# Kernel tuning notes

Hardware: AMD Instinct MI355X
Metric: run time of the kernel (lower is better)

Reference implementation:

```python
import jax, jax.numpy as jnp
import numpy as np

N, NOBJ, M, H, W = 512, 16, 8192, 128, 128


def _rand_rotations(key, n):
    A = jax.random.normal(key, (n, 3, 3), dtype=jnp.float32)
    q, r = jnp.linalg.qr(A)
    q = q * jnp.sign(jnp.diagonal(r, axis1=-2, axis2=-1))[:, None, :]
    det = jnp.linalg.det(q)  # +-1; flip first column if det == -1
    q = q.at[:, :, 0].multiply(det[:, None])
    return q


def setup_inputs() -> dict:
    key = jax.random.key(0)
    ks = jax.random.split(key, 10)
    obj_id = jax.random.randint(ks[0], (N,), 0, NOBJ, dtype=jnp.int32)
    # realistic pinhole intrinsics (pixels), slight per-sample jitter
    base_K = jnp.array([[600.0, 0.0, 64.0], [0.0, 600.0, 64.0], [0.0, 0.0, 1.0]], jnp.float32)
    cam_K = base_K[None] + jax.random.normal(ks[1], (N, 3, 3)) * jnp.array(
        [[5.0, 0.0, 1.0], [0.0, 5.0, 1.0], [0.0, 0.0, 0.0]], jnp.float32)
    gt_R = _rand_rotations(ks[2], N)
    # small rotational perturbation for pred
    pred_R = _rand_rotations(ks[3], N) @ gt_R
    gt_t = jnp.concatenate([jax.random.normal(ks[4], (N, 2)) * 20.0,
                            500.0 + jax.random.uniform(ks[4], (N, 1)) * 300.0], axis=-1)
    pred_t = gt_t + jax.random.normal(ks[5], (N, 3)) * 5.0
    mesh_points = jax.random.normal(ks[6], (NOBJ, M, 3)) * 50.0  # mm-scale meshes
    diameters = 150.0 + jax.random.uniform(ks[7], (NOBJ,)) * 150.0
    gt_coord_3d_roi = jax.random.normal(ks[8], (N, 3, H, W)) * 50.0
    gt_mask_vis_roi = jax.random.bernoulli(ks[9], 0.4, (N, 1, H, W))
    return dict(obj_id=obj_id, cam_K=cam_K, gt_cam_R_m2c=gt_R, gt_cam_t_m2c=gt_t,
                pred_cam_R_m2c=pred_R, pred_cam_t_m2c=pred_t,
                gt_coord_3d_roi=gt_coord_3d_roi, gt_mask_vis_roi=gt_mask_vis_roi,
                mesh_points=mesh_points, diameters=diameters)


def _project(K, x):
    # K: [N,3,3], x: [N,...,3] -> pixel coords [N,...,2]
    h = jnp.einsum('nij,n...j->n...i', K, x)
    return h[..., :2] / h[..., 2:3]


def reference(obj_id, cam_K, gt_cam_R_m2c, gt_cam_t_m2c, pred_cam_R_m2c,
              pred_cam_t_m2c, gt_coord_3d_roi, gt_mask_vis_roi, mesh_points, diameters):
    # RE (degrees)
    R_diff = pred_cam_R_m2c @ jnp.swapaxes(gt_cam_R_m2c, -2, -1)
    trace = R_diff[..., 0, 0] + R_diff[..., 1, 1] + R_diff[..., 2, 2]
    re = jnp.arccos((jnp.clip(trace, -1.0, 3.0) - 1.0) * 0.5) * (180.0 / jnp.pi)
    # TE (cm)
    te = jnp.linalg.norm(pred_cam_t_m2c - gt_cam_t_m2c, axis=-1) * 100.0
    # ADD: mean distance between transformed mesh points, / diameter
    pts = mesh_points[obj_id]                      # [N,M,3]
    dR = pred_cam_R_m2c - gt_cam_R_m2c
    dt = pred_cam_t_m2c - gt_cam_t_m2c
    diff = jnp.einsum('nij,nmj->nmi', dR, pts) + dt[:, None, :]
    ad = jnp.linalg.norm(diff, axis=-1).mean(axis=-1) / diameters[obj_id]
    # PROJ: mean projected distance over mesh points
    xp = jnp.einsum('nij,nmj->nmi', pred_cam_R_m2c, pts) + pred_cam_t_m2c[:, None, :]
    xg = jnp.einsum('nij,nmj->nmi', gt_cam_R_m2c, pts) + gt_cam_t_m2c[:, None, :]
    pj = jnp.linalg.norm(_project(cam_K, xp) - _project(cam_K, xg), axis=-1).mean(axis=-1)
    # PROJ-visible: same over visible ROI pixels (masked mean instead of ragged gather)
    verts = jnp.transpose(gt_coord_3d_roi, (0, 2, 3, 1))  # [N,H,W,3]
    vp = jnp.einsum('nij,nhwj->nhwi', pred_cam_R_m2c, verts) + pred_cam_t_m2c[:, None, None, :]
    vg = jnp.einsum('nij,nhwj->nhwi', gt_cam_R_m2c, verts) + gt_cam_t_m2c[:, None, None, :]
    d = jnp.linalg.norm(_project(cam_K, vp) - _project(cam_K, vg), axis=-1)  # [N,H,W]
    mask = gt_mask_vis_roi[:, 0].astype(d.dtype)
    pv = (d * mask).sum(axis=(1, 2)) / jnp.maximum(mask.sum(axis=(1, 2)), 1.0)
    return re, te, ad, pj, pv
```

## Files before the change

kernel.cpp:

```cpp
#include <hip/hip_runtime.h>
#include <math.h>

#define NS   512
#define NOBJ 16
#define MPTS 8192
#define HH   128
#define WW   128
#define HW   (HH * WW)
#define BLOCK 1024
#define NWAVE (BLOCK / 64)

__device__ __forceinline__ float frcp(float x)  { return __builtin_amdgcn_rcpf(x); }
__device__ __forceinline__ float fsqrt(float x) { return __builtin_amdgcn_sqrtf(x); }

__global__ __launch_bounds__(BLOCK) void score_kernel(
    const int*   __restrict__ obj_id,
    const float* __restrict__ cam_K,
    const float* __restrict__ gt_R,
    const float* __restrict__ gt_t,
    const float* __restrict__ pr_R,
    const float* __restrict__ pr_t,
    const float* __restrict__ coord,
    const int*   __restrict__ mask,
    const float* __restrict__ mesh,
    const float* __restrict__ diam,
    float*       __restrict__ out)
{
    const int n   = blockIdx.x;
    const int tid = threadIdx.x;

    float K[9], Rg[9], Rp[9], tg[3], tp[3];
#pragma unroll
    for (int i = 0; i < 9; ++i) {
        K[i]  = cam_K[n * 9 + i];
        Rg[i] = gt_R [n * 9 + i];
        Rp[i] = pr_R [n * 9 + i];
    }
#pragma unroll
    for (int i = 0; i < 3; ++i) {
        tg[i] = gt_t[n * 3 + i];
        tp[i] = pr_t[n * 3 + i];
    }
    const int   obj = obj_id[n];
    const float dia = diam[obj];

    float dR[9], dt[3];
#pragma unroll
    for (int i = 0; i < 9; ++i) dR[i] = Rp[i] - Rg[i];
#pragma unroll
    for (int i = 0; i < 3; ++i) dt[i] = tp[i] - tg[i];

    float Ap[9], Ag[9], bp[3], bg[3];
#pragma unroll
    for (int r = 0; r < 3; ++r) {
#pragma unroll
        for (int c = 0; c < 3; ++c) {
            Ap[r * 3 + c] = K[r * 3 + 0] * Rp[0 * 3 + c]
                          + K[r * 3 + 1] * Rp[1 * 3 + c]
                          + K[r * 3 + 2] * Rp[2 * 3 + c];
            Ag[r * 3 + c] = K[r * 3 + 0] * Rg[0 * 3 + c]
                          + K[r * 3 + 1] * Rg[1 * 3 + c]
                          + K[r * 3 + 2] * Rg[2 * 3 + c];
        }
        bp[r] = K[r * 3 + 0] * tp[0] + K[r * 3 + 1] * tp[1] + K[r * 3 + 2] * tp[2];
        bg[r] = K[r * 3 + 0] * tg[0] + K[r * 3 + 1] * tg[1] + K[r * 3 + 2] * tg[2];
    }

    float s_ad = 0.0f, s_pj = 0.0f;

    const float4* mp4 = (const float4*)(mesh + (size_t)obj * MPTS * 3);
#pragma unroll
    for (int it = 0; it < MPTS / (BLOCK * 4); ++it) {
        const int k = it * BLOCK + tid;
        const float4 f0 = mp4[k * 3 + 0];
        const float4 f1 = mp4[k * 3 + 1];
        const float4 f2 = mp4[k * 3 + 2];
        const float px[4] = {f0.x, f0.w, f1.z, f2.y};
        const float py[4] = {f0.y, f1.x, f1.w, f2.z};
        const float pz[4] = {f0.z, f1.y, f2.x, f2.w};
#pragma unroll
        for (int j = 0; j < 4; ++j) {
            const float x = px[j], y = py[j], z = pz[j];
            const float dx = fmaf(dR[0], x, fmaf(dR[1], y, fmaf(dR[2], z, dt[0])));
            const float dy = fmaf(dR[3], x, fmaf(dR[4], y, fmaf(dR[5], z, dt[1])));
            const float dz = fmaf(dR[6], x, fmaf(dR[7], y, fmaf(dR[8], z, dt[2])));
            s_ad += fsqrt(fmaf(dx, dx, fmaf(dy, dy, dz * dz)));
            const float hpx = fmaf(Ap[0], x, fmaf(Ap[1], y, fmaf(Ap[2], z, bp[0])));
            const float hpy = fmaf(Ap[3], x, fmaf(Ap[4], y, fmaf(Ap[5], z, bp[1])));
            const float hpz = fmaf(Ap[6], x, fmaf(Ap[7], y, fmaf(Ap[8], z, bp[2])));
            const float hgx = fmaf(Ag[0], x, fmaf(Ag[1], y, fmaf(Ag[2], z, bg[0])));
            const float hgy = fmaf(Ag[3], x, fmaf(Ag[4], y, fmaf(Ag[5], z, bg[1])));
            const float hgz = fmaf(Ag[6], x, fmaf(Ag[7], y, fmaf(Ag[8], z, bg[2])));
            const float iwp = frcp(hpz), iwg = frcp(hgz);
            const float du = fmaf(hpx, iwp, -hgx * iwg);
            const float dv = fmaf(hpy, iwp, -hgy * iwg);
            s_pj += fsqrt(fmaf(du, du, dv * dv));
        }
    }

    const float* cx = coord + (size_t)n * 3 * HW;
    const int*   mk = mask + (size_t)n * HW;
    const float4* cx4 = (const float4*)cx;
    const float4* cy4 = (const float4*)(cx + HW);
    const float4* cz4 = (const float4*)(cx + 2 * HW);
    const int4*   mk4 = (const int4*)mk;

    float s_pv = 0.0f, s_m = 0.0f;
#pragma unroll
    for (int it = 0; it < HW / 4 / BLOCK; ++it) {
        const int p = it * BLOCK + tid;
        const float4 vx = cx4[p];
        const float4 vy = cy4[p];
        const float4 vz = cz4[p];
        const int4   mm = mk4[p];

        const float xs[4] = {vx.x, vx.y, vx.z, vx.w};
        const float ys[4] = {vy.x, vy.y, vy.z, vy.w};
        const float zs[4] = {vz.x, vz.y, vz.z, vz.w};
        const int   ms[4] = {mm.x, mm.y, mm.z, mm.w};

#pragma unroll
        for (int j = 0; j < 4; ++j) {
            const float x = xs[j], y = ys[j], z = zs[j];
            const float hpx = fmaf(Ap[0], x, fmaf(Ap[1], y, fmaf(Ap[2], z, bp[0])));
            const float hpy = fmaf(Ap[3], x, fmaf(Ap[4], y, fmaf(Ap[5], z, bp[1])));
            const float hpz = fmaf(Ap[6], x, fmaf(Ap[7], y, fmaf(Ap[8], z, bp[2])));
            const float hgx = fmaf(Ag[0], x, fmaf(Ag[1], y, fmaf(Ag[2], z, bg[0])));
            const float hgy = fmaf(Ag[3], x, fmaf(Ag[4], y, fmaf(Ag[5], z, bg[1])));
            const float hgz = fmaf(Ag[6], x, fmaf(Ag[7], y, fmaf(Ag[8], z, bg[2])));
            const float iwp = frcp(hpz), iwg = frcp(hgz);
            const float du = fmaf(hpx, iwp, -hgx * iwg);
            const float dv = fmaf(hpy, iwp, -hgy * iwg);
            const float d  = fsqrt(fmaf(du, du, dv * dv));
            const float fm = (ms[j] != 0) ? 1.0f : 0.0f;
            s_pv += d * fm;
            s_m  += fm;
        }
    }

    float vals[4] = {s_ad, s_pj, s_pv, s_m};
#pragma unroll
    for (int k = 0; k < 4; ++k) {
#pragma unroll
        for (int off = 32; off > 0; off >>= 1)
            vals[k] += __shfl_down(vals[k], off, 64);
    }

    __shared__ float red[4][NWAVE];
    const int wave = tid >> 6;
    const int lane = tid & 63;
    if (lane == 0) {
#pragma unroll
        for (int k = 0; k < 4; ++k) red[k][wave] = vals[k];
    }
    __syncthreads();

    if (tid == 0) {
        float tot[4];
#pragma unroll
        for (int k = 0; k < 4; ++k) {
            float s = 0.0f;
#pragma unroll
            for (int w = 0; w < NWAVE; ++w) s += red[k][w];
            tot[k] = s;
        }

        float trace = 0.0f;
#pragma unroll
        for (int i = 0; i < 9; ++i) trace += Rp[i] * Rg[i];
        trace = fminf(fmaxf(trace, -1.0f), 3.0f);
        const float re = acosf((trace - 1.0f) * 0.5f) * (180.0f / 3.14159265358979323846f);
        const float te = sqrtf(dt[0] * dt[0] + dt[1] * dt[1] + dt[2] * dt[2]) * 100.0f;

        out[0 * NS + n] = re;
        out[1 * NS + n] = te;
        out[2 * NS + n] = tot[0] * (1.0f / MPTS) / dia;
        out[3 * NS + n] = tot[1] * (1.0f / MPTS);
        out[4 * NS + n] = tot[2] / fmaxf(tot[3], 1.0f);
    }
}

extern "C" void kernel_launch(void* const* d_in, const int* in_sizes, int n_in,
                              void* d_out, int out_size, void* d_ws, size_t ws_size,
                              hipStream_t stream) {
    const int*   obj_id = (const int*)  d_in[0];
    const float* cam_K  = (const float*)d_in[1];
    const float* gt_R   = (const float*)d_in[2];
    const float* gt_t   = (const float*)d_in[3];
    const float* pr_R   = (const float*)d_in[4];
    const float* pr_t   = (const float*)d_in[5];
    const float* coord  = (const float*)d_in[6];
    const int*   mask   = (const int*)  d_in[7];
    const float* mesh   = (const float*)d_in[8];
    const float* diam   = (const float*)d_in[9];
    float* out = (float*)d_out;

    score_kernel<<<NS, BLOCK, 0, stream>>>(obj_id, cam_K, gt_R, gt_t, pr_R, pr_t,
                                           coord, mask, mesh, diam, out);
}
```

Baseline: 190.5 us.

## Split each sample across four smaller blocks with a second reduction kernel

Each sample's mesh and ROI work is split across four 256-thread blocks, giving 2048 blocks instead of 512 blocks of 1024 threads. Partial sums go to workspace, and a small second kernel combines them and writes the AD/PROJ/PROJ-visible outputs. Per-sample constants are made wave-uniform with readfirstlane so they can live in scalar registers. The intent is better occupancy, load balance and tail behaviour across CUs, at the cost of an extra launch and a workspace round trip.

Result: no change. 192.0 us (+0.8%).

```diff
diff --git a/kernel.cpp b/kernel.cpp
--- a/kernel.cpp
+++ b/kernel.cpp
@@ -1,19 +1,23 @@
 #include <hip/hip_runtime.h>
 #include <math.h>
 
-#define NS   512
-#define NOBJ 16
-#define MPTS 8192
-#define HH   128
-#define WW   128
-#define HW   (HH * WW)
-#define BLOCK 1024
+#define NS    512
+#define NOBJ  16
+#define MPTS  8192
+#define HH    128
+#define WW    128
+#define HW    (HH * WW)
+#define BLOCK 256
+#define SPLIT 4
 #define NWAVE (BLOCK / 64)
 
 __device__ __forceinline__ float frcp(float x)  { return __builtin_amdgcn_rcpf(x); }
 __device__ __forceinline__ float fsqrt(float x) { return __builtin_amdgcn_sqrtf(x); }
-
-__global__ __launch_bounds__(BLOCK) void score_kernel(
+__device__ __forceinline__ float rfl(float x) {
+    return __int_as_float(__builtin_amdgcn_readfirstlane(__float_as_int(x)));
+}
+
+__global__ __launch_bounds__(BLOCK) void score_partial(
     const int*   __restrict__ obj_id,
     const float* __restrict__ cam_K,
     const float* __restrict__ gt_R,
@@ -23,10 +27,12 @@
     const float* __restrict__ coord,
     const int*   __restrict__ mask,
     const float* __restrict__ mesh,
-    const float* __restrict__ diam,
+    float*       __restrict__ ws,
     float*       __restrict__ out)
 {
-    const int n   = blockIdx.x;
+    const int b   = blockIdx.x;
+    const int n   = b >> 2;
+    const int c   = b & (SPLIT - 1);
     const int tid = threadIdx.x;
 
     float K[9], Rg[9], Rp[9], tg[3], tp[3];
@@ -41,37 +47,44 @@
         tg[i] = gt_t[n * 3 + i];
         tp[i] = pr_t[n * 3 + i];
     }
-    const int   obj = obj_id[n];
-    const float dia = diam[obj];
-
-    float dR[9], dt[3];
-#pragma unroll
-    for (int i = 0; i < 9; ++i) dR[i] = Rp[i] - Rg[i];
-#pragma unroll
-    for (int i = 0; i < 3; ++i) dt[i] = tp[i] - tg[i];
-
-    float Ap[9], Ag[9], bp[3], bg[3];
+    const int obj = __builtin_amdgcn_readfirstlane(obj_id[n]);
+
+    if (c == 0 && tid == 0) {
+        float trace = 0.0f;
+#pragma unroll
+        for (int i = 0; i < 9; ++i) trace += Rp[i] * Rg[i];
+        trace = fminf(fmaxf(trace, -1.0f), 3.0f);
+        out[0 * NS + n] = acosf((trace - 1.0f) * 0.5f) * (180.0f / 3.14159265358979323846f);
+        const float dx = tp[0] - tg[0], dy = tp[1] - tg[1], dz = tp[2] - tg[2];
+        out[1 * NS + n] = sqrtf(dx * dx + dy * dy + dz * dz) * 100.0f;
+    }
+
+    float dR[9], dt[3], Ap[9], Ag[9], bp[3], bg[3];
+#pragma unroll
+    for (int i = 0; i < 9; ++i) dR[i] = rfl(Rp[i] - Rg[i]);
+#pragma unroll
+    for (int i = 0; i < 3; ++i) dt[i] = rfl(tp[i] - tg[i]);
 #pragma unroll
     for (int r = 0; r < 3; ++r) {
 #pragma unroll
-        for (int c = 0; c < 3; ++c) {
-            Ap[r * 3 + c] = K[r * 3 + 0] * Rp[0 * 3 + c]
-                          + K[r * 3 + 1] * Rp[1 * 3 + c]
-                          + K[r * 3 + 2] * Rp[2 * 3 + c];
-            Ag[r * 3 + c] = K[r * 3 + 0] * Rg[0 * 3 + c]
-                          + K[r * 3 + 1] * Rg[1 * 3 + c]
-                          + K[r * 3 + 2] * Rg[2 * 3 + c];
-        }
-        bp[r] = K[r * 3 + 0] * tp[0] + K[r * 3 + 1] * tp[1] + K[r * 3 + 2] * tp[2];
-        bg[r] = K[r * 3 + 0] * tg[0] + K[r * 3 + 1] * tg[1] + K[r * 3 + 2] * tg[2];
+        for (int col = 0; col < 3; ++col) {
+            Ap[r * 3 + col] = rfl(K[r * 3 + 0] * Rp[0 * 3 + col]
+                                + K[r * 3 + 1] * Rp[1 * 3 + col]
+                                + K[r * 3 + 2] * Rp[2 * 3 + col]);
+            Ag[r * 3 + col] = rfl(K[r * 3 + 0] * Rg[0 * 3 + col]
+                                + K[r * 3 + 1] * Rg[1 * 3 + col]
+                                + K[r * 3 + 2] * Rg[2 * 3 + col]);
+        }
+        bp[r] = rfl(K[r * 3 + 0] * tp[0] + K[r * 3 + 1] * tp[1] + K[r * 3 + 2] * tp[2]);
+        bg[r] = rfl(K[r * 3 + 0] * tg[0] + K[r * 3 + 1] * tg[1] + K[r * 3 + 2] * tg[2]);
     }
 
     float s_ad = 0.0f, s_pj = 0.0f;
 
     const float4* mp4 = (const float4*)(mesh + (size_t)obj * MPTS * 3);
 #pragma unroll
-    for (int it = 0; it < MPTS / (BLOCK * 4); ++it) {
-        const int k = it * BLOCK + tid;
+    for (int it = 0; it < MPTS / SPLIT / (BLOCK * 4); ++it) {
+        const int k = c * (MPTS / SPLIT / 4) + it * BLOCK + tid;
         const float4 f0 = mp4[k * 3 + 0];
         const float4 f1 = mp4[k * 3 + 1];
         const float4 f2 = mp4[k * 3 + 2];
@@ -99,26 +112,23 @@
     }
 
     const float* cx = coord + (size_t)n * 3 * HW;
-    const int*   mk = mask + (size_t)n * HW;
     const float4* cx4 = (const float4*)cx;
     const float4* cy4 = (const float4*)(cx + HW);
     const float4* cz4 = (const float4*)(cx + 2 * HW);
-    const int4*   mk4 = (const int4*)mk;
+    const int4*   mk4 = (const int4*)(mask + (size_t)n * HW);
 
     float s_pv = 0.0f, s_m = 0.0f;
 #pragma unroll
-    for (int it = 0; it < HW / 4 / BLOCK; ++it) {
-        const int p = it * BLOCK + tid;
+    for (int it = 0; it < HW / 4 / SPLIT / BLOCK; ++it) {
+        const int p = c * (HW / 4 / SPLIT) + it * BLOCK + tid;
         const float4 vx = cx4[p];
         const float4 vy = cy4[p];
         const float4 vz = cz4[p];
         const int4   mm = mk4[p];
-
         const float xs[4] = {vx.x, vx.y, vx.z, vx.w};
         const float ys[4] = {vy.x, vy.y, vy.z, vy.w};
         const float zs[4] = {vz.x, vz.y, vz.z, vz.w};
         const int   ms[4] = {mm.x, mm.y, mm.z, mm.w};
-
 #pragma unroll
         for (int j = 0; j < 4; ++j) {
             const float x = xs[j], y = ys[j], z = zs[j];
@@ -145,7 +155,6 @@
         for (int off = 32; off > 0; off >>= 1)
             vals[k] += __shfl_down(vals[k], off, 64);
     }
-
     __shared__ float red[4][NWAVE];
     const int wave = tid >> 6;
     const int lane = tid & 63;
@@ -154,30 +163,35 @@
         for (int k = 0; k < 4; ++k) red[k][wave] = vals[k];
     }
     __syncthreads();
-
     if (tid == 0) {
-        float tot[4];
 #pragma unroll
         for (int k = 0; k < 4; ++k) {
             float s = 0.0f;
 #pragma unroll
             for (int w = 0; w < NWAVE; ++w) s += red[k][w];
-            tot[k] = s;
-        }
-
-        float trace = 0.0f;
-#pragma unroll
-        for (int i = 0; i < 9; ++i) trace += Rp[i] * Rg[i];
-        trace = fminf(fmaxf(trace, -1.0f), 3.0f);
-        const float re = acosf((trace - 1.0f) * 0.5f) * (180.0f / 3.14159265358979323846f);
-        const float te = sqrtf(dt[0] * dt[0] + dt[1] * dt[1] + dt[2] * dt[2]) * 100.0f;
-
-        out[0 * NS + n] = re;
-        out[1 * NS + n] = te;
-        out[2 * NS + n] = tot[0] * (1.0f / MPTS) / dia;
-        out[3 * NS + n] = tot[1] * (1.0f / MPTS);
-        out[4 * NS + n] = tot[2] / fmaxf(tot[3], 1.0f);
-    }
+            ws[(size_t)(n * SPLIT + c) * 4 + k] = s;
+        }
+    }
+}
+
+__global__ __launch_bounds__(256) void score_reduce(
+    const float* __restrict__ ws,
+    const int*   __restrict__ obj_id,
+    const float* __restrict__ diam,
+    float*       __restrict__ out)
+{
+    const int n = blockIdx.x * blockDim.x + threadIdx.x;
+    if (n >= NS) return;
+    float ad = 0.0f, pj = 0.0f, pv = 0.0f, m = 0.0f;
+#pragma unroll
+    for (int cb = 0; cb < SPLIT; ++cb) {
+        const float* p = ws + (size_t)(n * SPLIT + cb) * 4;
+        ad += p[0]; pj += p[1]; pv += p[2]; m += p[3];
+    }
+    const float dia = diam[obj_id[n]];
+    out[2 * NS + n] = ad * (1.0f / MPTS) / dia;
+    out[3 * NS + n] = pj * (1.0f / MPTS);
+    out[4 * NS + n] = pv / fmaxf(m, 1.0f);
 }
 
 extern "C" void kernel_launch(void* const* d_in, const int* in_sizes, int n_in,
@@ -194,7 +208,9 @@
     const float* mesh   = (const float*)d_in[8];
     const float* diam   = (const float*)d_in[9];
     float* out = (float*)d_out;
-
-    score_kernel<<<NS, BLOCK, 0, stream>>>(obj_id, cam_K, gt_R, gt_t, pr_R, pr_t,
-                                           coord, mask, mesh, diam, out);
-}
+    float* ws  = (float*)d_ws;
+
+    score_partial<<<NS * SPLIT, BLOCK, 0, stream>>>(obj_id, cam_K, gt_R, gt_t, pr_R,
+                                                    pr_t, coord, mask, mesh, ws, out);
+    score_reduce<<<(NS + 255) / 256, 256, 0, stream>>>(ws, obj_id, diam, out);
+}
```
